# Optimization experiments

Measured on AMD Instinct MI355X. Metric: run time of the kernel, lower is better.

Reference implementation:

```python
import jax, jax.numpy as jnp
import numpy as np

B, T, E, H, D = 4, 1024, 1024, 16, 64


def rel_shift(x):
    # x: [B, H, T1, T2] -> Transformer-XL relative shift
    b, h, t1, t2 = x.shape
    x = jnp.pad(x, ((0, 0), (0, 0), (0, 0), (1, 0)))  # pad zeros on left of last dim
    x = x.reshape(b, h, t2 + 1, t1)[:, :, 1:]
    return x.reshape(b, h, t1, t2)


def setup_inputs() -> dict:
    key = jax.random.key(0)
    ks = jax.random.split(key, 9)
    s = 0.02
    return {
        "x": jax.random.normal(ks[0], (B, T, E), jnp.float32),
        "pos": jax.random.normal(ks[1], (1, T, E), jnp.float32),
        "Wq": jax.random.normal(ks[2], (E, H, D), jnp.float32) * s,
        "Wk": jax.random.normal(ks[3], (E, H, D), jnp.float32) * s,
        "Wv": jax.random.normal(ks[4], (E, H, D), jnp.float32) * s,
        "Wr": jax.random.normal(ks[5], (E, H, D), jnp.float32) * s,
        "r_w_bias": jax.random.normal(ks[6], (1, H, 1, D), jnp.float32) * s,
        "r_r_bias": jax.random.normal(ks[7], (1, H, 1, D), jnp.float32) * s,
        "merge_W": jax.random.normal(ks[8], (E, E), jnp.float32) * s,
        "merge_b": jnp.zeros((E,), jnp.float32),
    }


def reference(x, pos, Wq, Wk, Wv, Wr, r_w_bias, r_r_bias, merge_W, merge_b):
    d = Wq.shape[-1]
    scale = d ** -0.5
    # per-head linear projections via einsum (MultiHeadLinear)
    q = jnp.einsum('bte,ehd->bhtd', x, Wq) * scale   # [B,H,T,D]
    k = jnp.einsum('bte,ehd->bhtd', x, Wk)           # [B,H,T,D]
    v = jnp.einsum('bte,ehd->bhtd', x, Wv)           # [B,H,T,D]
    r = jnp.einsum('upe,ehd->uhpd', pos, Wr)[0]      # [H,P,D], P == T

    # content logits: (q + u) . k
    content_logits = jnp.einsum('bhtd,bhsd->bhts', q + r_w_bias, k)
    # relative logits: (q + v_bias) . rel_keys, then rel_shift
    relative_logits = jnp.einsum('bhtd,hpd->bhtp', q + r_r_bias, r)
    relative_logits = rel_shift(relative_logits)

    logits = content_logits + relative_logits        # [B,H,T,T]
    weights = jax.nn.softmax(logits, axis=-1)
    # attend and merge heads: [B,T,H,D] -> [B,T,E]
    attended = jnp.einsum('bhts,bhsd->bthd', weights, v).reshape(x.shape[0], x.shape[1], -1)
    return attended @ merge_W + merge_b
```

## Files before the change

### kernel.cpp

```cpp
#include <hip/hip_runtime.h>
#include <hip/hip_bf16.h>

#define BB 4
#define TT 1024
#define EE 1024
#define HH 16
#define DD 64

typedef unsigned short ushort_t;
typedef unsigned int uint_t;
typedef __attribute__((ext_vector_type(8))) short short8;
typedef __attribute__((ext_vector_type(4))) float f32x4;

__device__ __forceinline__ ushort_t f2bf(float f) {
  uint_t u = __float_as_uint(f);
  u += 0x7fffu + ((u >> 16) & 1u);
  return (ushort_t)(u >> 16);
}
__device__ __forceinline__ float bf2f(ushort_t s) {
  return __uint_as_float(((uint_t)s) << 16);
}

__device__ __forceinline__ void gload16(const ushort_t* src, ushort_t* dst) {
  __builtin_amdgcn_global_load_lds(
      (const __attribute__((address_space(1))) void*)src,
      (__attribute__((address_space(3))) void*)dst, 16, 0, 0);
}

__global__ void __launch_bounds__(256) conv_flat(
    const float* __restrict__ in, ushort_t* __restrict__ out, int n) {
  int i = (blockIdx.x * 256 + threadIdx.x) * 8;
  if (i >= n) return;
  float4 a = *(const float4*)(in + i);
  float4 b = *(const float4*)(in + i + 4);
  uint4 o;
  o.x = (uint_t)f2bf(a.x) | ((uint_t)f2bf(a.y) << 16);
  o.y = (uint_t)f2bf(a.z) | ((uint_t)f2bf(a.w) << 16);
  o.z = (uint_t)f2bf(b.x) | ((uint_t)f2bf(b.y) << 16);
  o.w = (uint_t)f2bf(b.z) | ((uint_t)f2bf(b.w) << 16);
  *(uint4*)(out + i) = o;
}

__global__ void __launch_bounds__(256) trans_conv4(
    const float* __restrict__ W0, const float* __restrict__ W1,
    const float* __restrict__ W2, const float* __restrict__ W3,
    ushort_t* __restrict__ O0, ushort_t* __restrict__ O1,
    ushort_t* __restrict__ O2, ushort_t* __restrict__ O3) {
  const float* W; ushort_t* Oh;
  switch (blockIdx.z) {
    case 0: W = W0; Oh = O0; break;
    case 1: W = W1; Oh = O1; break;
    case 2: W = W2; Oh = O2; break;
    default: W = W3; Oh = O3; break;
  }
  __shared__ float Ts[64][65];
  const int n0 = blockIdx.x * 64, k0 = blockIdx.y * 64;
  const int t = threadIdx.x;
  const int r = t >> 2, cs = (t & 3) * 16;
  const float* src = W + (size_t)(k0 + r) * 1024 + n0 + cs;
  #pragma unroll
  for (int e = 0; e < 16; e += 4) {
    float4 v4 = *(const float4*)(src + e);
    Ts[r][cs + e] = v4.x; Ts[r][cs + e + 1] = v4.y;
    Ts[r][cs + e + 2] = v4.z; Ts[r][cs + e + 3] = v4.w;
  }
  __syncthreads();
  ushort_t hb[16];
  #pragma unroll
  for (int e = 0; e < 16; e++) hb[e] = f2bf(Ts[cs + e][r]);
  ushort_t* dh = Oh + (size_t)(n0 + r) * 1024 + k0 + cs;
  *(uint4*)dh = *(const uint4*)hb;
  *(uint4*)(dh + 8) = *(const uint4*)(hb + 8);
}

__global__ void __launch_bounds__(256) trans_conv(
    const float* __restrict__ W, ushort_t* __restrict__ Oh,
    ushort_t* __restrict__ Ol) {
  __shared__ float Ts[64][65];
  const int n0 = blockIdx.x * 64, k0 = blockIdx.y * 64;
  const int t = threadIdx.x;
  const int r = t >> 2, cs = (t & 3) * 16;
  const float* src = W + (size_t)(k0 + r) * 1024 + n0 + cs;
  #pragma unroll
  for (int e = 0; e < 16; e += 4) {
    float4 v4 = *(const float4*)(src + e);
    Ts[r][cs + e] = v4.x; Ts[r][cs + e + 1] = v4.y;
    Ts[r][cs + e + 2] = v4.z; Ts[r][cs + e + 3] = v4.w;
  }
  __syncthreads();
  ushort_t hb[16], lb[16];
  #pragma unroll
  for (int e = 0; e < 16; e++) {
    float v = Ts[cs + e][r];
    hb[e] = f2bf(v);
    lb[e] = f2bf(v - bf2f(hb[e]));
  }
  ushort_t* dh = Oh + (size_t)(n0 + r) * 1024 + k0 + cs;
  *(uint4*)dh = *(const uint4*)hb;
  *(uint4*)(dh + 8) = *(const uint4*)(hb + 8);
  ushort_t* dl = Ol + (size_t)(n0 + r) * 1024 + k0 + cs;
  *(uint4*)dl = *(const uint4*)lb;
  *(uint4*)(dl + 8) = *(const uint4*)(lb + 8);
}

__global__ void __launch_bounds__(256) mfma_gemm_proj(
    const ushort_t* __restrict__ A,
    const ushort_t* __restrict__ B0, const ushort_t* __restrict__ B1,
    const ushort_t* __restrict__ B2,
    ushort_t* __restrict__ o_qu, ushort_t* __restrict__ o_qv,
    ushort_t* __restrict__ o_k, ushort_t* __restrict__ o_v,
    const float* __restrict__ bias_u, const float* __restrict__ bias_v,
    int mode) {
  __shared__ ushort_t sA[2][128 * 32];
  __shared__ ushort_t sB[2][128 * 32];
  const int tid = threadIdx.x;
  const int w = tid >> 6, lane = tid & 63, g = lane >> 4, cl = lane & 15;
  const int wr = w >> 1, wc = w & 1;

  int widx, n0l;
  const ushort_t* Bt;
  if (mode == 0) {
    widx = blockIdx.x >> 3;
    n0l = (blockIdx.x & 7) * 128;
    Bt = (widx == 0) ? B0 : ((widx == 1) ? B1 : B2);
  } else {
    widx = 3;
    n0l = blockIdx.x * 128;
    Bt = B0;
  }
  const int m0 = blockIdx.y * 128;

  f32x4 acc[4][4];
  #pragma unroll
  for (int fi = 0; fi < 4; fi++)
    #pragma unroll
    for (int fj = 0; fj < 4; fj++) acc[fi][fj] = (f32x4){0.f, 0.f, 0.f, 0.f};

  auto STAGE = [&](int buf, int t) {
    const int k0b = t * 64;
    #pragma unroll
    for (int i = 0; i < 2; i++) {
      int cb = w * 128 + i * 64;
      int c = cb + lane;
      const char* sa = (const char*)A + (size_t)(m0 + (c >> 2)) * 2048 + k0b + (c & 3) * 16;
      gload16((const ushort_t*)sa, &sA[buf][cb * 8]);
      const char* sb = (const char*)Bt + (size_t)(n0l + (c >> 2)) * 2048 + k0b + (c & 3) * 16;
      gload16((const ushort_t*)sb, &sB[buf][cb * 8]);
    }
  };

  STAGE(0, 0);
  __syncthreads();
  int cur = 0;
  for (int t = 0; t < 32; t++) {
    if (t + 1 < 32) STAGE(cur ^ 1, t + 1);
    short8 af[4], bfr[4];
    #pragma unroll
    for (int f = 0; f < 4; f++) {
      af[f] = *(const short8*)&sA[cur][(wr * 64 + f * 16 + cl) * 32 + g * 8];
      bfr[f] = *(const short8*)&sB[cur][(wc * 64 + f * 16 + cl) * 32 + g * 8];
    }
    #pragma unroll
    for (int fi = 0; fi < 4; fi++)
      #pragma unroll
      for (int fj = 0; fj < 4; fj++)
        acc[fi][fj] = __builtin_amdgcn_mfma_f32_16x16x32_bf16(af[fi], bfr[fj], acc[fi][fj], 0, 0, 0);
    __syncthreads();
    cur ^= 1;
  }

  #pragma unroll
  for (int fi = 0; fi < 4; fi++)
    #pragma unroll
    for (int fj = 0; fj < 4; fj++)
      #pragma unroll
      for (int reg = 0; reg < 4; reg++) {
        int m = m0 + wr * 64 + fi * 16 + 4 * g + reg;
        int n = n0l + wc * 64 + fj * 16 + cl;
        float val = acc[fi][fj][reg];
        int h = n >> 6, d = n & 63;
        if (mode == 0) {
          int b = m >> 10, tt = m & 1023;
          if (widx == 0) {
            size_t idx = (((size_t)(b * HH + h)) * TT + tt) * DD + d;
            float s = val * 0.125f;
            o_qu[idx] = f2bf(s + bias_u[n]);
            o_qv[idx] = f2bf(s + bias_v[n]);
          } else if (widx == 1) {
            size_t idx = (((size_t)(b * HH + h)) * TT + tt) * DD + d;
            o_k[idx] = f2bf(val);
          } else {
            size_t idx = (((size_t)(b * HH + h)) * DD + d) * TT + tt;
            o_v[idx] = f2bf(val);
          }
        } else {
          size_t idx = ((size_t)h * TT + m) * DD + d;
          o_qu[idx] = f2bf(val);
        }
      }
}

__global__ void __launch_bounds__(256) mfma_gemm_merge(
    const ushort_t* __restrict__ Ah, const ushort_t* __restrict__ Al,
    const ushort_t* __restrict__ Bh, const ushort_t* __restrict__ Bl,
    const float* __restrict__ bias, float* __restrict__ out) {
  __shared__ ushort_t sAh[2][128 * 32], sAl[2][128 * 32];
  __shared__ ushort_t sBh[2][128 * 32], sBl[2][128 * 32];
  const int tid = threadIdx.x;
  const int w = tid >> 6, lane = tid & 63, g = lane >> 4, cl = lane & 15;
  const int wr = w >> 1, wc = w & 1;
  const int n0l = blockIdx.x * 128;
  const int m0 = blockIdx.y * 128;

  f32x4 acc[4][4];
  #pragma unroll
  for (int fi = 0; fi < 4; fi++)
    #pragma unroll
    for (int fj = 0; fj < 4; fj++) acc[fi][fj] = (f32x4){0.f, 0.f, 0.f, 0.f};

  auto STAGE = [&](int buf, int t) {
    const int k0b = t * 64;
    #pragma unroll
    for (int i = 0; i < 2; i++) {
      int cb = w * 128 + i * 64;
      int c = cb + lane;
      size_t offA = (size_t)(m0 + (c >> 2)) * 2048 + k0b + (c & 3) * 16;
      size_t offB = (size_t)(n0l + (c >> 2)) * 2048 + k0b + (c & 3) * 16;
      gload16((const ushort_t*)((const char*)Ah + offA), &sAh[buf][cb * 8]);
      gload16((const ushort_t*)((const char*)Al + offA), &sAl[buf][cb * 8]);
      gload16((const ushort_t*)((const char*)Bh + offB), &sBh[buf][cb * 8]);
      gload16((const ushort_t*)((const char*)Bl + offB), &sBl[buf][cb * 8]);
    }
  };

  STAGE(0, 0);
  __syncthreads();
  int cur = 0;
  for (int t = 0; t < 32; t++) {
    if (t + 1 < 32) STAGE(cur ^ 1, t + 1);
    short8 ah[4], al[4], bh[4], bl[4];
    #pragma unroll
    for (int f = 0; f < 4; f++) {
      int ra = (wr * 64 + f * 16 + cl) * 32 + g * 8;
      int rb = (wc * 64 + f * 16 + cl) * 32 + g * 8;
      ah[f] = *(const short8*)&sAh[cur][ra];
      al[f] = *(const short8*)&sAl[cur][ra];
      bh[f] = *(const short8*)&sBh[cur][rb];
      bl[f] = *(const short8*)&sBl[cur][rb];
    }
    #pragma unroll
    for (int fi = 0; fi < 4; fi++)
      #pragma unroll
      for (int fj = 0; fj < 4; fj++) {
        acc[fi][fj] = __builtin_amdgcn_mfma_f32_16x16x32_bf16(ah[fi], bh[fj], acc[fi][fj], 0, 0, 0);
        acc[fi][fj] = __builtin_amdgcn_mfma_f32_16x16x32_bf16(al[fi], bh[fj], acc[fi][fj], 0, 0, 0);
        acc[fi][fj] = __builtin_amdgcn_mfma_f32_16x16x32_bf16(ah[fi], bl[fj], acc[fi][fj], 0, 0, 0);
      }
    __syncthreads();
    cur ^= 1;
  }

  #pragma unroll
  for (int fi = 0; fi < 4; fi++)
    #pragma unroll
    for (int fj = 0; fj < 4; fj++)
      #pragma unroll
      for (int reg = 0; reg < 4; reg++) {
        int m = m0 + wr * 64 + fi * 16 + 4 * g + reg;
        int n = n0l + wc * 64 + fj * 16 + cl;
        out[(size_t)m * 1024 + n] = acc[fi][fj][reg] + bias[n];
      }
}

__device__ __forceinline__ void stage8s(ushort_t* region, const ushort_t* grow0,
                                        int rstride, int r0, int lane) {
  int flat16 = r0 * 8 + lane;
  int row = flat16 >> 3;
  int ch = flat16 & 7;
  const ushort_t* src = grow0 + (size_t)row * rstride + ((((ch << 4) ^ ((row & 7) << 4))) >> 1);
  gload16(src, region + r0 * 64);
}

__device__ __forceinline__ short8 ldsw(const ushort_t* base, int row, int offB) {
  const char* p = (const char*)base + row * 128 + (offB ^ ((row & 7) << 4));
  return *(const short8*)p;
}

__global__ void __launch_bounds__(256) attn_mfma_kernel(
    const ushort_t* __restrict__ qu_g, const ushort_t* __restrict__ qv_g,
    const ushort_t* __restrict__ k_g, const ushort_t* __restrict__ vt_g,
    const ushort_t* __restrict__ r_g,
    ushort_t* __restrict__ att_h, ushort_t* __restrict__ att_l)
{
    __shared__ ushort_t sK[4][64 * 64];
    __shared__ ushort_t sG[4][2304];

    const int tid = threadIdx.x;
    const int w = tid >> 6;
    const int lane = tid & 63;
    const int g = lane >> 4;
    const int cl = lane & 15;

    const int lid = blockIdx.x + 16 * blockIdx.y + 256 * blockIdx.z;
    const int xcd = lid & 7, seq = lid >> 3;
    const int bhg = xcd * 8 + (seq >> 4);
    const int i0 = (seq & 15) * 64;
    const int h = bhg & 15;
    const int b = bhg >> 4;
    const size_t base_bh = ((size_t)(b * HH + h)) * TT * DD;
    const ushort_t* rh = r_g + (size_t)h * TT * DD;

    ushort_t* sKw = sK[w];
    ushort_t* Gw = sG[w];
    ushort_t* Pb = sG[w];

    const int qrow = i0 + 16 * w + cl;
    const ushort_t* qup = qu_g + base_bh + (size_t)qrow * 64;
    short8 aQ0 = *(const short8*)(qup + 8 * g);
    short8 aQ1 = *(const short8*)(qup + 32 + 8 * g);
    const ushort_t* qv1p = qv_g + base_bh + (size_t)qrow * 64;
    short8 aV0 = *(const short8*)(qv1p + 8 * g);
    short8 aV1 = *(const short8*)(qv1p + 32 + 8 * g);
    int r2row = qrow + 1; if (r2row > 1023) r2row = 1023;
    const ushort_t* qv2p = qv_g + base_bh + (size_t)r2row * 64;
    short8 aV0s = *(const short8*)(qv2p + 8 * g);
    short8 aV1s = *(const short8*)(qv2p + 32 + 8 * g);

    auto STAGE = [&](int jt16) {
      const ushort_t* kb = k_g + base_bh + (size_t)(jt16 * 64) * 64;
      #pragma unroll
      for (int r0 = 0; r0 < 64; r0 += 8)
        stage8s(sKw, kb, 64, r0, lane);
    };

    auto RLD = [&](int base, int s, short8& A, short8& B) {
      const ushort_t* rp = rh + (size_t)(base + s * 16 + cl) * 64 + 8 * g;
      A = *(const short8*)rp;
      B = *(const short8*)(rp + 32);
    };
    auto GST = [&](int s, short8 A, short8 B, short8 X0, short8 X1) {
      f32x4 ga = (f32x4){0.f, 0.f, 0.f, 0.f};
      ga = __builtin_amdgcn_mfma_f32_16x16x32_bf16(X0, A, ga, 0, 0, 0);
      ga = __builtin_amdgcn_mfma_f32_16x16x32_bf16(X1, B, ga, 0, 0, 0);
      int m = s * 16 + cl;
      *(uint_t*)(Gw + m * 18 + 4 * g) =
          (uint_t)f2bf(ga[0]) | ((uint_t)f2bf(ga[1]) << 16);
      *(uint_t*)(Gw + m * 18 + 4 * g + 2) =
          (uint_t)f2bf(ga[2]) | ((uint_t)f2bf(ga[3]) << 16);
    };

    f32x4 Oa[4];
    #pragma unroll
    for (int q = 0; q < 4; q++) Oa[q] = (f32x4){0.f, 0.f, 0.f, 0.f};
    float lrun[4] = {0.f, 0.f, 0.f, 0.f};

    for (int jt16 = 0; jt16 < 16; jt16++) {
        const int j0 = jt16 * 64;
        const int dji = j0 - i0;

        STAGE(jt16);
        asm volatile("s_waitcnt vmcnt(0)" ::: "memory");
        __builtin_amdgcn_sched_barrier(0);

        f32x4 sacc[4];
        #pragma unroll
        for (int jt = 0; jt < 4; jt++) sacc[jt] = (f32x4){0.f, 0.f, 0.f, 0.f};
        __builtin_amdgcn_s_setprio(1);
        #pragma unroll
        for (int jt = 0; jt < 4; jt++) {
            int krow = jt * 16 + cl;
            short8 b0 = ldsw(sKw, krow, 16 * g);
            short8 b1 = ldsw(sKw, krow, 64 + 16 * g);
            sacc[jt] = __builtin_amdgcn_mfma_f32_16x16x32_bf16(aQ0, b0, sacc[jt], 0, 0, 0);
            sacc[jt] = __builtin_amdgcn_mfma_f32_16x16x32_bf16(aQ1, b1, sacc[jt], 0, 0, 0);
        }
        __builtin_amdgcn_s_setprio(0);

        if (dji < 0) {
            const int cbase1w = 1008 + dji - 16 * w;
            short8 a0, b0, a1, b1, a2, b2;
            RLD(cbase1w, 0, a0, b0);
            RLD(cbase1w, 1, a1, b1);
            RLD(cbase1w, 2, a2, b2);
            GST(0, a0, b0, aV0, aV1); RLD(cbase1w, 3, a0, b0);
            GST(1, a1, b1, aV0, aV1); RLD(cbase1w, 4, a1, b1);
            GST(2, a2, b2, aV0, aV1);
            GST(3, a0, b0, aV0, aV1);
            GST(4, a1, b1, aV0, aV1);
            #pragma unroll
            for (int jt = 0; jt < 4; jt++)
                #pragma unroll
                for (int reg = 0; reg < 4; reg++) {
                    int m1p = 15 + jt * 16 + cl - 4 * g - reg;
                    sacc[jt][reg] += bf2f(Gw[m1p * 18 + 4 * g + reg]);
                }
        } else if (dji > 0) {
            int rbase2w = dji - 17 - 16 * w;
            if (rbase2w < 0) rbase2w = 0;
            short8 a0, b0, a1, b1, a2, b2;
            RLD(rbase2w, 0, a0, b0);
            RLD(rbase2w, 1, a1, b1);
            RLD(rbase2w, 2, a2, b2);
            GST(0, a0, b0, aV0s, aV1s); RLD(rbase2w, 3, a0, b0);
            GST(1, a1, b1, aV0s, aV1s); RLD(rbase2w, 4, a1, b1);
            GST(2, a2, b2, aV0s, aV1s);
            GST(3, a0, b0, aV0s, aV1s);
            GST(4, a1, b1, aV0s, aV1s);
            #pragma unroll
            for (int jt = 0; jt < 4; jt++)
                #pragma unroll
                for (int reg = 0; reg < 4; reg++) {
                    int dlt = dji + jt * 16 + cl - 16 * w - 4 * g - reg;
                    int idx2 = dlt - 2 - rbase2w;
                    if (dlt >= 2) sacc[jt][reg] += bf2f(Gw[idx2 * 18 + 4 * g + reg]);
                }
        } else {
            ushort_t* Gw2 = Gw + 64 * 18;
            for (int sub = 0; sub < 4; sub++) {
                int m = sub * 16 + cl;
                const ushort_t* rp = rh + (size_t)(960 + m) * 64 + 8 * g;
                f32x4 gacc = (f32x4){0.f, 0.f, 0.f, 0.f};
                gacc = __builtin_amdgcn_mfma_f32_16x16x32_bf16(aV0, *(const short8*)rp, gacc, 0, 0, 0);
                gacc = __builtin_amdgcn_mfma_f32_16x16x32_bf16(aV1, *(const short8*)(rp + 32), gacc, 0, 0, 0);
                *(uint_t*)(Gw + m * 18 + 4 * g) =
                    (uint_t)f2bf(gacc[0]) | ((uint_t)f2bf(gacc[1]) << 16);
                *(uint_t*)(Gw + m * 18 + 4 * g + 2) =
                    (uint_t)f2bf(gacc[2]) | ((uint_t)f2bf(gacc[3]) << 16);
            }
            for (int sub = 0; sub < 4; sub++) {
                int m = sub * 16 + cl;
                const ushort_t* rp = rh + (size_t)m * 64 + 8 * g;
                f32x4 gacc = (f32x4){0.f, 0.f, 0.f, 0.f};
                gacc = __builtin_amdgcn_mfma_f32_16x16x32_bf16(aV0s, *(const short8*)rp, gacc, 0, 0, 0);
                gacc = __builtin_amdgcn_mfma_f32_16x16x32_bf16(aV1s, *(const short8*)(rp + 32), gacc, 0, 0, 0);
                *(uint_t*)(Gw2 + m * 18 + 4 * g) =
                    (uint_t)f2bf(gacc[0]) | ((uint_t)f2bf(gacc[1]) << 16);
                *(uint_t*)(Gw2 + m * 18 + 4 * g + 2) =
                    (uint_t)f2bf(gacc[2]) | ((uint_t)f2bf(gacc[3]) << 16);
            }
            #pragma unroll
            for (int jt = 0; jt < 4; jt++)
                #pragma unroll
                for (int reg = 0; reg < 4; reg++) {
                    int m1 = 63 + jt * 16 + cl - 16 * w - 4 * g - reg;
                    if (m1 <= 63) sacc[jt][reg] += bf2f(Gw[m1 * 18 + 4 * g + reg]);
                }
            #pragma unroll
            for (int jt = 0; jt < 4; jt++)
                #pragma unroll
                for (int reg = 0; reg < 4; reg++) {
                    int dlt = jt * 16 + cl - 16 * w - 4 * g - reg;
                    if (dlt >= 2) sacc[jt][reg] += bf2f(Gw2[(dlt - 2) * 18 + 4 * g + reg]);
                }
        }

        #pragma unroll
        for (int reg = 0; reg < 4; reg++) {
            #pragma unroll
            for (int jt = 0; jt < 4; jt++) {
                float p = __expf(sacc[jt][reg]);
                lrun[reg] += p;
                Pb[(4 * g + reg) * 72 + jt * 16 + cl] = f2bf(p);
            }
        }

        __builtin_amdgcn_s_setprio(1);
        #pragma unroll
        for (int kk = 0; kk < 2; kk++) {
            short8 aP = *(const short8*)((const char*)Pb + cl * 144 + 64 * kk + 16 * g);
            #pragma unroll
            for (int q = 0; q < 4; q++) {
                const ushort_t* vp = vt_g + base_bh + (size_t)(q * 16 + cl) * 1024
                                     + j0 + kk * 32 + 8 * g;
                short8 bV = *(const short8*)vp;
                Oa[q] = __builtin_amdgcn_mfma_f32_16x16x32_bf16(aP, bV, Oa[q], 0, 0, 0);
            }
        }
        __builtin_amdgcn_s_setprio(0);
    }

    float inv[4];
    #pragma unroll
    for (int reg = 0; reg < 4; reg++) {
        float s = lrun[reg];
        #pragma unroll
        for (int msk = 1; msk <= 8; msk <<= 1) s += __shfl_xor(s, msk);
        inv[reg] = 1.f / s;
    }
    #pragma unroll
    for (int q = 0; q < 4; q++)
        #pragma unroll
        for (int reg = 0; reg < 4; reg++) {
            int i = i0 + 16 * w + 4 * g + reg;
            int d = q * 16 + cl;
            float val = Oa[q][reg] * inv[reg];
            ushort_t hi = f2bf(val);
            ushort_t lo = f2bf(val - bf2f(hi));
            size_t oi = (((size_t)(b * TT + i)) * HH + h) * DD + d;
            att_h[oi] = hi;
            att_l[oi] = lo;
        }
}

extern "C" void kernel_launch(void* const* d_in, const int* in_sizes, int n_in,
                              void* d_out, int out_size, void* d_ws, size_t ws_size,
                              hipStream_t stream) {
    const float* x    = (const float*)d_in[0];
    const float* pos  = (const float*)d_in[1];
    const float* Wq   = (const float*)d_in[2];
    const float* Wk   = (const float*)d_in[3];
    const float* Wv   = (const float*)d_in[4];
    const float* Wr   = (const float*)d_in[5];
    const float* ub   = (const float*)d_in[6];
    const float* vb   = (const float*)d_in[7];
    const float* mW   = (const float*)d_in[8];
    const float* mb   = (const float*)d_in[9];
    float* out = (float*)d_out;

    const size_t M1 = 1u << 20;
    ushort_t* ws = (ushort_t*)d_ws;
    ushort_t* xb   = ws;
    ushort_t* posb = ws + 4 * M1;
    ushort_t* wqt  = ws + 5 * M1;
    ushort_t* wkt  = ws + 6 * M1;
    ushort_t* wvt  = ws + 7 * M1;
    ushort_t* wrt  = ws + 8 * M1;
    ushort_t* wmh  = ws + 9 * M1;
    ushort_t* wml  = ws + 10 * M1;
    ushort_t* qu_g = ws + 11 * M1;
    ushort_t* qv_g = ws + 15 * M1;
    ushort_t* k_g  = ws + 19 * M1;
    ushort_t* vt_g = ws + 23 * M1;
    ushort_t* r_g  = ws + 27 * M1;
    ushort_t* ath  = ws + 28 * M1;
    ushort_t* atl  = ws + 32 * M1;

    dim3 blk(256);

    hipLaunchKernelGGL(conv_flat, dim3(2048), blk, 0, stream, x, xb, 4194304);
    hipLaunchKernelGGL(conv_flat, dim3(512), blk, 0, stream, pos, posb, 1048576);
    hipLaunchKernelGGL(trans_conv4, dim3(16, 16, 4), blk, 0, stream,
                       Wq, Wk, Wv, Wr, wqt, wkt, wvt, wrt);
    hipLaunchKernelGGL(trans_conv, dim3(16, 16), blk, 0, stream, mW, wmh, wml);

    hipLaunchKernelGGL(mfma_gemm_proj, dim3(24, 32), blk, 0, stream,
                       xb, wqt, wkt, wvt, qu_g, qv_g, k_g, vt_g, ub, vb, 0);
    hipLaunchKernelGGL(mfma_gemm_proj, dim3(8, 8), blk, 0, stream,
                       posb, wrt, wrt, wrt, r_g, r_g, r_g, r_g, ub, vb, 1);

    hipLaunchKernelGGL(attn_mfma_kernel, dim3(TT / 64, HH, BB), blk, 0, stream,
                       qu_g, qv_g, k_g, vt_g, r_g, ath, atl);

    hipLaunchKernelGGL(mfma_gemm_merge, dim3(8, 32), blk, 0, stream,
                       ath, atl, wmh, wml, mb, out);
}
```

Measured before the change: 307.8 us.

## Merge prep and projection launches, drop merge-weight low split, prefetch V

Three changes. The two input conversions become one launch, the five weight transposes become one launch, and the x-side and pos-side projection GEMMs run in a single grid whose pos-side blocks exit early past row 1024. The merge GEMM drops the low-order bf16 part of the merge weight, removing one third of its MFMAs and one of its shared-memory streams at the cost of merge precision. In the attention kernel, the V fragments are loaded earlier in each iteration so that global-load latency overlaps with the logit computation.

```diff
diff --git a/kernel.cpp b/kernel.cpp
--- a/kernel.cpp
+++ b/kernel.cpp
@@ -27,10 +27,15 @@
       (__attribute__((address_space(3))) void*)dst, 16, 0, 0);
 }
 
-__global__ void __launch_bounds__(256) conv_flat(
-    const float* __restrict__ in, ushort_t* __restrict__ out, int n) {
-  int i = (blockIdx.x * 256 + threadIdx.x) * 8;
-  if (i >= n) return;
+__global__ void __launch_bounds__(256) conv_flat2(
+    const float* __restrict__ x, const float* __restrict__ pos,
+    ushort_t* __restrict__ ox, ushort_t* __restrict__ opos) {
+  int bid = blockIdx.x;
+  const float* in;
+  ushort_t* out;
+  int i;
+  if (bid < 2048) { in = x; out = ox; i = (bid * 256 + threadIdx.x) * 8; }
+  else { in = pos; out = opos; i = ((bid - 2048) * 256 + threadIdx.x) * 8; }
   float4 a = *(const float4*)(in + i);
   float4 b = *(const float4*)(in + i + 4);
   uint4 o;
@@ -41,17 +46,20 @@
   *(uint4*)(out + i) = o;
 }
 
-__global__ void __launch_bounds__(256) trans_conv4(
+__global__ void __launch_bounds__(256) trans_conv5(
     const float* __restrict__ W0, const float* __restrict__ W1,
     const float* __restrict__ W2, const float* __restrict__ W3,
+    const float* __restrict__ W4,
     ushort_t* __restrict__ O0, ushort_t* __restrict__ O1,
-    ushort_t* __restrict__ O2, ushort_t* __restrict__ O3) {
+    ushort_t* __restrict__ O2, ushort_t* __restrict__ O3,
+    ushort_t* __restrict__ O4) {
   const float* W; ushort_t* Oh;
   switch (blockIdx.z) {
     case 0: W = W0; Oh = O0; break;
     case 1: W = W1; Oh = O1; break;
     case 2: W = W2; Oh = O2; break;
-    default: W = W3; Oh = O3; break;
+    case 3: W = W3; Oh = O3; break;
+    default: W = W4; Oh = O4; break;
   }
   __shared__ float Ts[64][65];
   const int n0 = blockIdx.x * 64, k0 = blockIdx.y * 64;
@@ -73,44 +81,14 @@
   *(uint4*)(dh + 8) = *(const uint4*)(hb + 8);
 }
 
-__global__ void __launch_bounds__(256) trans_conv(
-    const float* __restrict__ W, ushort_t* __restrict__ Oh,
-    ushort_t* __restrict__ Ol) {
-  __shared__ float Ts[64][65];
-  const int n0 = blockIdx.x * 64, k0 = blockIdx.y * 64;
-  const int t = threadIdx.x;
-  const int r = t >> 2, cs = (t & 3) * 16;
-  const float* src = W + (size_t)(k0 + r) * 1024 + n0 + cs;
-  #pragma unroll
-  for (int e = 0; e < 16; e += 4) {
-    float4 v4 = *(const float4*)(src + e);
-    Ts[r][cs + e] = v4.x; Ts[r][cs + e + 1] = v4.y;
-    Ts[r][cs + e + 2] = v4.z; Ts[r][cs + e + 3] = v4.w;
-  }
-  __syncthreads();
-  ushort_t hb[16], lb[16];
-  #pragma unroll
-  for (int e = 0; e < 16; e++) {
-    float v = Ts[cs + e][r];
-    hb[e] = f2bf(v);
-    lb[e] = f2bf(v - bf2f(hb[e]));
-  }
-  ushort_t* dh = Oh + (size_t)(n0 + r) * 1024 + k0 + cs;
-  *(uint4*)dh = *(const uint4*)hb;
-  *(uint4*)(dh + 8) = *(const uint4*)(hb + 8);
-  ushort_t* dl = Ol + (size_t)(n0 + r) * 1024 + k0 + cs;
-  *(uint4*)dl = *(const uint4*)lb;
-  *(uint4*)(dl + 8) = *(const uint4*)(lb + 8);
-}
-
 __global__ void __launch_bounds__(256) mfma_gemm_proj(
-    const ushort_t* __restrict__ A,
+    const ushort_t* __restrict__ Ax, const ushort_t* __restrict__ Ap,
     const ushort_t* __restrict__ B0, const ushort_t* __restrict__ B1,
-    const ushort_t* __restrict__ B2,
+    const ushort_t* __restrict__ B2, const ushort_t* __restrict__ B3,
     ushort_t* __restrict__ o_qu, ushort_t* __restrict__ o_qv,
     ushort_t* __restrict__ o_k, ushort_t* __restrict__ o_v,
-    const float* __restrict__ bias_u, const float* __restrict__ bias_v,
-    int mode) {
+    ushort_t* __restrict__ o_r,
+    const float* __restrict__ bias_u, const float* __restrict__ bias_v) {
   __shared__ ushort_t sA[2][128 * 32];
   __shared__ ushort_t sB[2][128 * 32];
   const int tid = threadIdx.x;
@@ -119,16 +97,20 @@
 
   int widx, n0l;
   const ushort_t* Bt;
-  if (mode == 0) {
+  const ushort_t* A;
+  if (blockIdx.x < 24) {
     widx = blockIdx.x >> 3;
     n0l = (blockIdx.x & 7) * 128;
     Bt = (widx == 0) ? B0 : ((widx == 1) ? B1 : B2);
+    A = Ax;
   } else {
     widx = 3;
-    n0l = blockIdx.x * 128;
-    Bt = B0;
+    n0l = (blockIdx.x - 24) * 128;
+    Bt = B3;
+    A = Ap;
   }
   const int m0 = blockIdx.y * 128;
+  if (widx == 3 && m0 >= 1024) return;
 
   f32x4 acc[4][4];
   #pragma unroll
@@ -179,33 +161,33 @@
         int n = n0l + wc * 64 + fj * 16 + cl;
         float val = acc[fi][fj][reg];
         int h = n >> 6, d = n & 63;
-        if (mode == 0) {
+        if (widx == 0) {
           int b = m >> 10, tt = m & 1023;
-          if (widx == 0) {
-            size_t idx = (((size_t)(b * HH + h)) * TT + tt) * DD + d;
-            float s = val * 0.125f;
-            o_qu[idx] = f2bf(s + bias_u[n]);
-            o_qv[idx] = f2bf(s + bias_v[n]);
-          } else if (widx == 1) {
-            size_t idx = (((size_t)(b * HH + h)) * TT + tt) * DD + d;
-            o_k[idx] = f2bf(val);
-          } else {
-            size_t idx = (((size_t)(b * HH + h)) * DD + d) * TT + tt;
-            o_v[idx] = f2bf(val);
-          }
+          size_t idx = (((size_t)(b * HH + h)) * TT + tt) * DD + d;
+          float s = val * 0.125f;
+          o_qu[idx] = f2bf(s + bias_u[n]);
+          o_qv[idx] = f2bf(s + bias_v[n]);
+        } else if (widx == 1) {
+          int b = m >> 10, tt = m & 1023;
+          size_t idx = (((size_t)(b * HH + h)) * TT + tt) * DD + d;
+          o_k[idx] = f2bf(val);
+        } else if (widx == 2) {
+          int b = m >> 10, tt = m & 1023;
+          size_t idx = (((size_t)(b * HH + h)) * DD + d) * TT + tt;
+          o_v[idx] = f2bf(val);
         } else {
           size_t idx = ((size_t)h * TT + m) * DD + d;
-          o_qu[idx] = f2bf(val);
+          o_r[idx] = f2bf(val);
         }
       }
 }
 
 __global__ void __launch_bounds__(256) mfma_gemm_merge(
     const ushort_t* __restrict__ Ah, const ushort_t* __restrict__ Al,
-    const ushort_t* __restrict__ Bh, const ushort_t* __restrict__ Bl,
+    const ushort_t* __restrict__ Bh,
     const float* __restrict__ bias, float* __restrict__ out) {
   __shared__ ushort_t sAh[2][128 * 32], sAl[2][128 * 32];
-  __shared__ ushort_t sBh[2][128 * 32], sBl[2][128 * 32];
+  __shared__ ushort_t sBh[2][128 * 32];
   const int tid = threadIdx.x;
   const int w = tid >> 6, lane = tid & 63, g = lane >> 4, cl = lane & 15;
   const int wr = w >> 1, wc = w & 1;
@@ -229,7 +211,6 @@
       gload16((const ushort_t*)((const char*)Ah + offA), &sAh[buf][cb * 8]);
       gload16((const ushort_t*)((const char*)Al + offA), &sAl[buf][cb * 8]);
       gload16((const ushort_t*)((const char*)Bh + offB), &sBh[buf][cb * 8]);
-      gload16((const ushort_t*)((const char*)Bl + offB), &sBl[buf][cb * 8]);
     }
   };
 
@@ -238,7 +219,7 @@
   int cur = 0;
   for (int t = 0; t < 32; t++) {
     if (t + 1 < 32) STAGE(cur ^ 1, t + 1);
-    short8 ah[4], al[4], bh[4], bl[4];
+    short8 ah[4], al[4], bh[4];
     #pragma unroll
     for (int f = 0; f < 4; f++) {
       int ra = (wr * 64 + f * 16 + cl) * 32 + g * 8;
@@ -246,7 +227,6 @@
       ah[f] = *(const short8*)&sAh[cur][ra];
       al[f] = *(const short8*)&sAl[cur][ra];
       bh[f] = *(const short8*)&sBh[cur][rb];
-      bl[f] = *(const short8*)&sBl[cur][rb];
     }
     #pragma unroll
     for (int fi = 0; fi < 4; fi++)
@@ -254,7 +234,6 @@
       for (int fj = 0; fj < 4; fj++) {
         acc[fi][fj] = __builtin_amdgcn_mfma_f32_16x16x32_bf16(ah[fi], bh[fj], acc[fi][fj], 0, 0, 0);
         acc[fi][fj] = __builtin_amdgcn_mfma_f32_16x16x32_bf16(al[fi], bh[fj], acc[fi][fj], 0, 0, 0);
-        acc[fi][fj] = __builtin_amdgcn_mfma_f32_16x16x32_bf16(ah[fi], bl[fj], acc[fi][fj], 0, 0, 0);
       }
     __syncthreads();
     cur ^= 1;
@@ -309,6 +288,7 @@
     const int b = bhg >> 4;
     const size_t base_bh = ((size_t)(b * HH + h)) * TT * DD;
     const ushort_t* rh = r_g + (size_t)h * TT * DD;
+    const ushort_t* vtb = vt_g + base_bh;
 
     ushort_t* sKw = sK[w];
     ushort_t* Gw = sG[w];
@@ -359,6 +339,10 @@
         const int dji = j0 - i0;
 
         STAGE(jt16);
+        short8 vA = *(const short8*)(vtb + (size_t)(0 * 16 + cl) * 1024 + j0 + 8 * g);
+        short8 vB = *(const short8*)(vtb + (size_t)(1 * 16 + cl) * 1024 + j0 + 8 * g);
+        short8 vC = *(const short8*)(vtb + (size_t)(2 * 16 + cl) * 1024 + j0 + 8 * g);
+        short8 vD = *(const short8*)(vtb + (size_t)(3 * 16 + cl) * 1024 + j0 + 8 * g);
         asm volatile("s_waitcnt vmcnt(0)" ::: "memory");
         __builtin_amdgcn_sched_barrier(0);
 
@@ -375,6 +359,11 @@
             sacc[jt] = __builtin_amdgcn_mfma_f32_16x16x32_bf16(aQ1, b1, sacc[jt], 0, 0, 0);
         }
         __builtin_amdgcn_s_setprio(0);
+
+        short8 vE = *(const short8*)(vtb + (size_t)(0 * 16 + cl) * 1024 + j0 + 32 + 8 * g);
+        short8 vF = *(const short8*)(vtb + (size_t)(1 * 16 + cl) * 1024 + j0 + 32 + 8 * g);
+        short8 vG = *(const short8*)(vtb + (size_t)(2 * 16 + cl) * 1024 + j0 + 32 + 8 * g);
+        short8 vH = *(const short8*)(vtb + (size_t)(3 * 16 + cl) * 1024 + j0 + 32 + 8 * g);
 
         if (dji < 0) {
             const int cbase1w = 1008 + dji - 16 * w;
@@ -465,16 +454,17 @@
         }
 
         __builtin_amdgcn_s_setprio(1);
-        #pragma unroll
-        for (int kk = 0; kk < 2; kk++) {
-            short8 aP = *(const short8*)((const char*)Pb + cl * 144 + 64 * kk + 16 * g);
-            #pragma unroll
-            for (int q = 0; q < 4; q++) {
-                const ushort_t* vp = vt_g + base_bh + (size_t)(q * 16 + cl) * 1024
-                                     + j0 + kk * 32 + 8 * g;
-                short8 bV = *(const short8*)vp;
-                Oa[q] = __builtin_amdgcn_mfma_f32_16x16x32_bf16(aP, bV, Oa[q], 0, 0, 0);
-            }
+        {
+            short8 aP0 = *(const short8*)((const char*)Pb + cl * 144 + 16 * g);
+            Oa[0] = __builtin_amdgcn_mfma_f32_16x16x32_bf16(aP0, vA, Oa[0], 0, 0, 0);
+            Oa[1] = __builtin_amdgcn_mfma_f32_16x16x32_bf16(aP0, vB, Oa[1], 0, 0, 0);
+            Oa[2] = __builtin_amdgcn_mfma_f32_16x16x32_bf16(aP0, vC, Oa[2], 0, 0, 0);
+            Oa[3] = __builtin_amdgcn_mfma_f32_16x16x32_bf16(aP0, vD, Oa[3], 0, 0, 0);
+            short8 aP1 = *(const short8*)((const char*)Pb + cl * 144 + 64 + 16 * g);
+            Oa[0] = __builtin_amdgcn_mfma_f32_16x16x32_bf16(aP1, vE, Oa[0], 0, 0, 0);
+            Oa[1] = __builtin_amdgcn_mfma_f32_16x16x32_bf16(aP1, vF, Oa[1], 0, 0, 0);
+            Oa[2] = __builtin_amdgcn_mfma_f32_16x16x32_bf16(aP1, vG, Oa[2], 0, 0, 0);
+            Oa[3] = __builtin_amdgcn_mfma_f32_16x16x32_bf16(aP1, vH, Oa[3], 0, 0, 0);
         }
         __builtin_amdgcn_s_setprio(0);
     }
@@ -526,7 +516,6 @@
     ushort_t* wvt  = ws + 7 * M1;
     ushort_t* wrt  = ws + 8 * M1;
     ushort_t* wmh  = ws + 9 * M1;
-    ushort_t* wml  = ws + 10 * M1;
     ushort_t* qu_g = ws + 11 * M1;
     ushort_t* qv_g = ws + 15 * M1;
     ushort_t* k_g  = ws + 19 * M1;
@@ -537,20 +526,17 @@
 
     dim3 blk(256);
 
-    hipLaunchKernelGGL(conv_flat, dim3(2048), blk, 0, stream, x, xb, 4194304);
-    hipLaunchKernelGGL(conv_flat, dim3(512), blk, 0, stream, pos, posb, 1048576);
-    hipLaunchKernelGGL(trans_conv4, dim3(16, 16, 4), blk, 0, stream,
-                       Wq, Wk, Wv, Wr, wqt, wkt, wvt, wrt);
-    hipLaunchKernelGGL(trans_conv, dim3(16, 16), blk, 0, stream, mW, wmh, wml);
-
-    hipLaunchKernelGGL(mfma_gemm_proj, dim3(24, 32), blk, 0, stream,
-                       xb, wqt, wkt, wvt, qu_g, qv_g, k_g, vt_g, ub, vb, 0);
-    hipLaunchKernelGGL(mfma_gemm_proj, dim3(8, 8), blk, 0, stream,
-                       posb, wrt, wrt, wrt, r_g, r_g, r_g, r_g, ub, vb, 1);
+    hipLaunchKernelGGL(conv_flat2, dim3(2560), blk, 0, stream, x, pos, xb, posb);
+    hipLaunchKernelGGL(trans_conv5, dim3(16, 16, 5), blk, 0, stream,
+                       Wq, Wk, Wv, Wr, mW, wqt, wkt, wvt, wrt, wmh);
+
+    hipLaunchKernelGGL(mfma_gemm_proj, dim3(32, 32), blk, 0, stream,
+                       xb, posb, wqt, wkt, wvt, wrt,
+                       qu_g, qv_g, k_g, vt_g, r_g, ub, vb);
 
     hipLaunchKernelGGL(attn_mfma_kernel, dim3(TT / 64, HH, BB), blk, 0, stream,
                        qu_g, qv_g, k_g, vt_g, r_g, ath, atl);
 
     hipLaunchKernelGGL(mfma_gemm_merge, dim3(8, 32), blk, 0, stream,
-                       ath, atl, wmh, wml, mb, out);
-}
+                       ath, atl, wmh, mb, out);
+}
```

New measurement: 362.6 us. +17.8%, slower.
